# Performance work log

Hardware: AMD Instinct MI355X
Metric: run time of the kernel (lower is better)

## Reference

```python
import jax, jax.numpy as jnp
import numpy as np

N_HEADS = 16

def setup_inputs() -> dict:
    key = jax.random.key(0)
    k1, k2, k3 = jax.random.split(key, 3)
    d = 1024
    x = jax.random.normal(k1, (2, 2048, d), dtype=jnp.float32)
    W_in = jax.random.normal(k2, (d, 3 * d), dtype=jnp.float32) * (d ** -0.5)
    W_out = jax.random.normal(k3, (d, d), dtype=jnp.float32) * (d ** -0.5)
    return {"x": x, "W_in": W_in, "W_out": W_out}

def reference(x, W_in, W_out):
    B, S, D = x.shape
    H = N_HEADS
    Dh = D // H
    qkv = x @ W_in                                  # [B,S,3D]
    q, k, v = jnp.split(qkv, 3, axis=-1)
    # [B,S,D] -> [B,H,S,Dh]
    q = q.reshape(B, S, H, Dh).transpose(0, 2, 1, 3)
    k = k.reshape(B, S, H, Dh).transpose(0, 2, 1, 3)
    v = v.reshape(B, S, H, Dh).transpose(0, 2, 1, 3)
    scores = jnp.einsum('bhqd,bhkd->bhqk', q, k)    # [B,H,S,S]
    causal = jnp.triu(jnp.ones((S, S), dtype=bool), k=1)
    scores = jnp.where(causal, -jnp.inf, scores)
    scores = scores / jnp.sqrt(jnp.asarray(Dh, scores.dtype))
    attn = jax.nn.softmax(scores, axis=-1)
    out = jnp.einsum('bhqk,bhkd->bhqd', attn, v)    # [B,H,S,Dh]
    out = out.transpose(0, 2, 1, 3).reshape(B, S, D)
    return out @ W_out
```

## Files before the change

### kernel.cpp

```cpp
#include <hip/hip_runtime.h>
#include <cstdint>
#include <cstddef>

typedef __bf16 bf16;
typedef bf16  bf16x4  __attribute__((ext_vector_type(4)));
typedef bf16  bf16x8  __attribute__((ext_vector_type(8)));
typedef float floatx4 __attribute__((ext_vector_type(4)));

#define BATCH 2
#define SEQ   2048
#define DIM   1024
#define NH    16
#define DH    64
#define D3    3072
#define MROWS 4096

__device__ __forceinline__ void gld16(void* lds, const void* gptr) {
  __builtin_amdgcn_global_load_lds(
      (const __attribute__((address_space(1))) unsigned int*)gptr,
      (__attribute__((address_space(3))) unsigned int*)lds, 16, 0, 0);
}

__global__ __launch_bounds__(256) void k_prep(const float4* __restrict__ x,
                                              bf16* __restrict__ xb,
                                              const float* __restrict__ Wi,
                                              bf16* __restrict__ wti,
                                              const float* __restrict__ Wo,
                                              bf16* __restrict__ wto) {
  __shared__ float tile[32][33];
  const int bid = blockIdx.x;
  if (bid < 4096) {
    int i = bid * 256 + threadIdx.x;
    float4 v = x[i];
    bf16x4 o;
    o.x = (bf16)v.x; o.y = (bf16)v.y; o.z = (bf16)v.z; o.w = (bf16)v.w;
    *(bf16x4*)(xb + (size_t)i * 4) = o;
    return;
  }
  const float* W; bf16* Wt; int N, id;
  if (bid < 7168) { W = Wi; Wt = wti; N = 3072; id = bid - 4096; }
  else            { W = Wo; Wt = wto; N = 1024; id = bid - 7168; }
  const int nb = N / 32;
  int n0 = (id % nb) * 32, k0 = (id / nb) * 32;
  int tx = threadIdx.x & 31, ty = threadIdx.x >> 5;
#pragma unroll
  for (int i = 0; i < 4; i++)
    tile[ty + i * 8][tx] = W[(size_t)(k0 + ty + i * 8) * N + n0 + tx];
  __syncthreads();
#pragma unroll
  for (int i = 0; i < 4; i++)
    Wt[(size_t)(n0 + ty + i * 8) * 1024 + k0 + tx] = (bf16)tile[tx][ty + i * 8];
}

__global__ __launch_bounds__(512, 2) void k_gemm256(const bf16* __restrict__ A,
                                                    const bf16* __restrict__ Bt,
                                                    bf16* __restrict__ qk,
                                                    bf16* __restrict__ vt) {
  constexpr int K = DIM;
  constexpr int nk = K / 64;
  __shared__ __align__(16) bf16 As[2][256 * 64];
  __shared__ __align__(16) bf16 Bs[2][256 * 64];

  const int t = threadIdx.x, l = t & 63, w = t >> 6;
  const int q = l >> 4, mm = l & 15;
  const int wm = w >> 2, wn = w & 3;

  int id = blockIdx.x;
  id = (id & 7) * 24 + (id >> 3);
  const int by = id / 12, bx = id % 12;
  const int m0 = by * 256, n0 = bx * 256;

  auto stA = [&](int T, int up) {
    const int bp = T & 1;
#pragma unroll
    for (int i = 0; i < 2; i++) {
      int c = t + i * 512;
      int row = ((c >> 9) << 7) + (up << 6) + ((c >> 3) & 63);
      int pos = c & 7;
      int gs = pos ^ (row & 7);
      gld16((char*)(As[bp] + row * 64 + pos * 8),
            A + (size_t)(m0 + row) * K + T * 64 + gs * 8);
    }
  };
  auto stB = [&](int T, int up) {
    const int bp = T & 1;
#pragma unroll
    for (int i = 0; i < 2; i++) {
      int c = t + i * 512;
      int row = ((c >> 8) << 6) + (up << 5) + ((c >> 3) & 31);
      int pos = c & 7;
      int gs = pos ^ (row & 7);
      gld16((char*)(Bs[bp] + row * 64 + pos * 8),
            Bt + (size_t)(n0 + row) * K + T * 64 + gs * 8);
    }
  };

  floatx4 acc[8][4] = {};

  stA(0, 0); stB(0, 0); stA(0, 1); stB(0, 1);
  stA(1, 0); stB(1, 0);

  for (int T = 0; T < nk; T++) {
    const int bp = T & 1;
    if (T + 1 < nk)
      asm volatile("s_waitcnt vmcnt(4)\n\ts_barrier" ::: "memory");
    else
      asm volatile("s_waitcnt vmcnt(0)\n\ts_barrier" ::: "memory");

    const bf16* Ab = As[bp] + (size_t)(wm * 128) * 64;
    const bf16* Bb = Bs[bp] + (size_t)(wn * 64) * 64;
    bf16x8 af[4][2], bf0[2][2], bf1[2][2];

    if (T + 1 < nk) stA(T + 1, 1);
#pragma unroll
    for (int mt = 0; mt < 4; mt++)
#pragma unroll
      for (int kk = 0; kk < 2; kk++)
        af[mt][kk] = *(const bf16x8*)(Ab + (size_t)(mt * 16 + mm) * 64 +
                                      ((kk * 4 + q) ^ (mm & 7)) * 8);
#pragma unroll
    for (int nt = 0; nt < 2; nt++)
#pragma unroll
      for (int kk = 0; kk < 2; kk++)
        bf0[nt][kk] = *(const bf16x8*)(Bb + (size_t)(nt * 16 + mm) * 64 +
                                       ((kk * 4 + q) ^ (mm & 7)) * 8);
    asm volatile("s_barrier" ::: "memory");
    __builtin_amdgcn_s_setprio(1);
#pragma unroll
    for (int mt = 0; mt < 4; mt++)
#pragma unroll
      for (int nt = 0; nt < 2; nt++)
#pragma unroll
        for (int kk = 0; kk < 2; kk++)
          acc[mt][nt] = __builtin_amdgcn_mfma_f32_16x16x32_bf16(
              af[mt][kk], bf0[nt][kk], acc[mt][nt], 0, 0, 0);
    __builtin_amdgcn_s_setprio(0);
    asm volatile("s_barrier" ::: "memory");

    if (T + 1 < nk) stB(T + 1, 1);
#pragma unroll
    for (int nt = 0; nt < 2; nt++)
#pragma unroll
      for (int kk = 0; kk < 2; kk++)
        bf1[nt][kk] = *(const bf16x8*)(Bb + (size_t)(32 + nt * 16 + mm) * 64 +
                                       ((kk * 4 + q) ^ (mm & 7)) * 8);
    asm volatile("s_barrier" ::: "memory");
    __builtin_amdgcn_s_setprio(1);
#pragma unroll
    for (int mt = 0; mt < 4; mt++)
#pragma unroll
      for (int nt = 0; nt < 2; nt++)
#pragma unroll
        for (int kk = 0; kk < 2; kk++)
          acc[mt][2 + nt] = __builtin_amdgcn_mfma_f32_16x16x32_bf16(
              af[mt][kk], bf1[nt][kk], acc[mt][2 + nt], 0, 0, 0);
    __builtin_amdgcn_s_setprio(0);
    asm volatile("s_barrier" ::: "memory");

    if (T + 2 < nk) stA(T + 2, 0);
#pragma unroll
    for (int mt = 0; mt < 4; mt++)
#pragma unroll
      for (int kk = 0; kk < 2; kk++)
        af[mt][kk] = *(const bf16x8*)(Ab + (size_t)(64 + mt * 16 + mm) * 64 +
                                      ((kk * 4 + q) ^ (mm & 7)) * 8);
    asm volatile("s_barrier" ::: "memory");
    __builtin_amdgcn_s_setprio(1);
#pragma unroll
    for (int mt = 0; mt < 4; mt++)
#pragma unroll
      for (int nt = 0; nt < 2; nt++)
#pragma unroll
        for (int kk = 0; kk < 2; kk++)
          acc[4 + mt][nt] = __builtin_amdgcn_mfma_f32_16x16x32_bf16(
              af[mt][kk], bf0[nt][kk], acc[4 + mt][nt], 0, 0, 0);
    __builtin_amdgcn_s_setprio(0);
    asm volatile("s_barrier" ::: "memory");

    if (T + 2 < nk) stB(T + 2, 0);
    asm volatile("s_barrier" ::: "memory");
    __builtin_amdgcn_s_setprio(1);
#pragma unroll
    for (int mt = 0; mt < 4; mt++)
#pragma unroll
      for (int nt = 0; nt < 2; nt++)
#pragma unroll
        for (int kk = 0; kk < 2; kk++)
          acc[4 + mt][2 + nt] = __builtin_amdgcn_mfma_f32_16x16x32_bf16(
              af[mt][kk], bf1[nt][kk], acc[4 + mt][2 + nt], 0, 0, 0);
    __builtin_amdgcn_s_setprio(0);
  }

#pragma unroll
  for (int mt = 0; mt < 8; mt++)
#pragma unroll
    for (int nt = 0; nt < 4; nt++) {
      int row = m0 + wm * 128 + mt * 16 + q * 4;
      int col = n0 + wn * 64 + nt * 16 + mm;
      if (col < 2048) {
#pragma unroll
        for (int r = 0; r < 4; r++)
          qk[(size_t)(row + r) * 2048 + col] = (bf16)acc[mt][nt][r];
      } else {
        int d = col - 2048;
        int hh = d >> 6, dh = d & 63;
#pragma unroll
        for (int r = 0; r < 4; r++) {
          int rr = row + r;
          int bb = rr >> 11, s = rr & 2047;
          vt[((size_t)(bb * 16 + hh) * 64 + dh) * SEQ + s] = (bf16)acc[mt][nt][r];
        }
      }
    }
}

template <typename OutT, int MODE, int BN>
__global__ __launch_bounds__(256) void k_gemm_bt(const bf16* __restrict__ A,
                                                 const bf16* __restrict__ Bt,
                                                 OutT* __restrict__ C,
                                                 bf16* __restrict__ qk,
                                                 bf16* __restrict__ vt,
                                                 int M, int N, int K) {
  constexpr int LN = 2 + BN / 64;
  __shared__ __align__(16) bf16 As[3][128 * 32];
  __shared__ __align__(16) bf16 Bs[3][BN * 32];
  const int t = threadIdx.x, l = t & 63, w = t >> 6;
  const int q = l >> 4, mm = l & 15;
  const int m0 = blockIdx.y * 128, n0 = blockIdx.x * BN;
  constexpr int MT = (BN == 128) ? 4 : 2;
  const int mo = (BN == 128) ? ((w >> 1) * 64) : (w * 32);
  const int no = (BN == 128) ? ((w & 1) * 64) : 0;
  const int sw = (mm >> 1) & 3;

  auto stage = [&](int kt) {
    const int bp = kt % 3;
#pragma unroll
    for (int i = 0; i < 2; i++) {
      int c = t + i * 256;
      int row = c >> 2, pos = c & 3;
      int gs = pos ^ ((row >> 1) & 3);
      gld16((char*)As[bp] + (size_t)c * 16, A + (size_t)(m0 + row) * K + kt * 32 + gs * 8);
    }
#pragma unroll
    for (int i = 0; i < BN / 64; i++) {
      int c = t + i * 256;
      int row = c >> 2, pos = c & 3;
      int gs = pos ^ ((row >> 1) & 3);
      gld16((char*)Bs[bp] + (size_t)c * 16, Bt + (size_t)(n0 + row) * K + kt * 32 + gs * 8);
    }
  };

  floatx4 acc[MT][4] = {};
  const int nk = K >> 5;

  stage(0);
  stage(1);

  for (int kt = 0; kt < nk; kt++) {
    if (kt + 1 < nk)
      asm volatile("s_waitcnt vmcnt(%0)\n\ts_barrier" :: "n"(LN) : "memory");
    else
      asm volatile("s_waitcnt vmcnt(0)\n\ts_barrier" ::: "memory");
    if (kt + 2 < nk) stage(kt + 2);

    const bf16* Ab = As[kt % 3];
    const bf16* Bb = Bs[kt % 3];
    bf16x8 af[MT], bfr[4];
#pragma unroll
    for (int mt = 0; mt < MT; mt++)
      af[mt] = *(const bf16x8*)(Ab + (size_t)(mo + mt * 16 + mm) * 32 + (q ^ sw) * 8);
#pragma unroll
    for (int nt = 0; nt < 4; nt++)
      bfr[nt] = *(const bf16x8*)(Bb + (size_t)(no + nt * 16 + mm) * 32 + (q ^ sw) * 8);
#pragma unroll
    for (int mt = 0; mt < MT; mt++)
#pragma unroll
      for (int nt = 0; nt < 4; nt++)
        acc[mt][nt] = __builtin_amdgcn_mfma_f32_16x16x32_bf16(af[mt], bfr[nt],
                                                              acc[mt][nt], 0, 0, 0);
  }
#pragma unroll
  for (int mt = 0; mt < MT; mt++)
#pragma unroll
    for (int nt = 0; nt < 4; nt++)
#pragma unroll
      for (int r = 0; r < 4; r++) {
        int row = m0 + mo + mt * 16 + q * 4 + r;
        int col = n0 + no + nt * 16 + mm;
        if (MODE == 0) {
          C[(size_t)row * N + col] = (OutT)acc[mt][nt][r];
        } else {
          if (col < 2048) {
            qk[(size_t)row * 2048 + col] = (bf16)acc[mt][nt][r];
          } else {
            int d = col - 2048;
            int hh = d >> 6, dh = d & 63;
            int bb = row >> 11, s = row & 2047;
            vt[((size_t)(bb * 16 + hh) * 64 + dh) * SEQ + s] = (bf16)acc[mt][nt][r];
          }
        }
      }
}

__global__ __launch_bounds__(256, 4) void k_attn(const bf16* __restrict__ qk,
                                                 const bf16* __restrict__ vt,
                                                 bf16* __restrict__ out) {
  const int bx = blockIdx.x;
  const int qt = 31 - (bx >> 5);
  const int bh = bx & 31;
  const int b = bh >> 4, h = bh & 15;
  const int t = threadIdx.x, l = t & 63, w = t >> 6;
  const int q4 = l >> 4, mm = l & 15;
  const int sw = (mm >> 1) & 3;

  __shared__ __align__(16) char lds[8192 + 16384 + 16384];
  bf16* Qs = (bf16*)lds;
  bf16* Ps = (bf16*)lds;
  bf16* Ks = (bf16*)(lds + 8192);
  bf16* Vs = (bf16*)(lds + 8192 + 16384);

  const size_t qkbase = (size_t)b * SEQ * 2048;
  const size_t vtbase = (size_t)bh * 64 * SEQ;

  auto stage = [&](int kt) {
    const int bp = kt & 1;
#pragma unroll
    for (int i = 0; i < 2; i++) {
      int row = t >> 2, pos = t & 3;
      int g = pos ^ ((row >> 1) & 3);
      gld16((char*)(Ks + bp * 4096) + ((size_t)t + i * 256) * 16,
            qk + qkbase + (size_t)(kt * 64 + row) * 2048 + 1024 + h * 64 + i * 32 + g * 8);
    }
#pragma unroll
    for (int i = 0; i < 2; i++) {
      int c = t + i * 256;
      int vr = c >> 3, vc = c & 7;
      int src = vc ^ (vr & 7);
      gld16((char*)(Vs + bp * 4096) + (size_t)c * 16,
            vt + vtbase + (size_t)vr * SEQ + kt * 64 + src * 8);
    }
  };

  {
    int row = t >> 2, col = (t & 3) * 8;
#pragma unroll
    for (int i = 0; i < 2; i++)
      gld16((char*)Qs + ((size_t)t + i * 256) * 16,
            qk + qkbase + (size_t)(qt * 64 + row) * 2048 + h * 64 + i * 32 + col);
  }
  stage(0);
  __syncthreads();
  bf16x8 qf[2];
#pragma unroll
  for (int ks = 0; ks < 2; ks++) {
    qf[ks] = *(const bf16x8*)(Qs + (size_t)(ks * 64 + w * 16 + mm) * 32 + q4 * 8);
#pragma unroll
    for (int j = 0; j < 8; j++)
      qf[ks][j] = (bf16)((float)qf[ks][j] * 0.18033688f);
  }
  __syncthreads();

  float l_i = 0.f;
  floatx4 oaccT[4] = {};
  const int qloc = w * 16 + mm;
  const float FM = 24.0f;

  bf16* Pw = Ps + (size_t)w * 640;

  for (int kt = 0; kt <= qt; kt++) {
    if (kt < qt) stage(kt + 1);
    const bf16* Kb = Ks + (kt & 1) * 4096;
    const bf16* Vb = Vs + (kt & 1) * 4096;

    floatx4 sacc[4] = {};
#pragma unroll
    for (int ks = 0; ks < 2; ks++)
#pragma unroll
      for (int ct = 0; ct < 4; ct++) {
        bf16x8 kf = *(const bf16x8*)(Kb + (size_t)(ks * 64 + ct * 16 + mm) * 32 + (q4 ^ sw) * 8);
        sacc[ct] = __builtin_amdgcn_mfma_f32_16x16x32_bf16(kf, qf[ks], sacc[ct], 0, 0, 0);
      }

    bf16x4 pk[4];
    float rsum = 0.f;
    if (kt == qt) {
#pragma unroll
      for (int ct = 0; ct < 4; ct++)
#pragma unroll
        for (int r = 0; r < 4; r++) {
          float e = (ct * 16 + q4 * 4 + r > qloc)
                        ? 0.f : __builtin_amdgcn_exp2f(sacc[ct][r] - FM);
          pk[ct][r] = (bf16)e;
          rsum += e;
        }
    } else {
#pragma unroll
      for (int ct = 0; ct < 4; ct++)
#pragma unroll
        for (int r = 0; r < 4; r++) {
          float e = __builtin_amdgcn_exp2f(sacc[ct][r] - FM);
          pk[ct][r] = (bf16)e;
          rsum += e;
        }
    }
    rsum += __shfl_xor(rsum, 16, 64);
    rsum += __shfl_xor(rsum, 32, 64);
    l_i += rsum;

#pragma unroll
    for (int ks = 0; ks < 2; ks++) {
      *(bf16x4*)(Pw + (size_t)mm * 40 + q4 * 4)      = pk[ks * 2 + 0];
      *(bf16x4*)(Pw + (size_t)mm * 40 + 16 + q4 * 4) = pk[ks * 2 + 1];
      bf16x8 pf = *(const bf16x8*)(Pw + (size_t)mm * 40 + q4 * 8);
#pragma unroll
      for (int nt = 0; nt < 4; nt++) {
        int chunk = (ks * 4 + q4) ^ (mm & 7);
        bf16x8 vf = *(const bf16x8*)(Vb + (size_t)(nt * 16 + mm) * 64 + chunk * 8);
        oaccT[nt] = __builtin_amdgcn_mfma_f32_16x16x32_bf16(vf, pf, oaccT[nt], 0, 0, 0);
      }
    }

    if (kt < qt) __syncthreads();
  }

  float inv = 1.0f / l_i;
  int qrow = qt * 64 + qloc;
  bf16* orow = out + ((size_t)b * SEQ + qrow) * DIM + h * 64;
#pragma unroll
  for (int nt = 0; nt < 4; nt++) {
    bf16x4 o4;
#pragma unroll
    for (int r = 0; r < 4; r++) o4[r] = (bf16)(oaccT[nt][r] * inv);
    *(bf16x4*)(orow + nt * 16 + q4 * 4) = o4;
  }
}

extern "C" void kernel_launch(void* const* d_in, const int* in_sizes, int n_in,
                              void* d_out, int out_size, void* d_ws, size_t ws_size,
                              hipStream_t stream) {
  const float* x     = (const float*)d_in[0];
  const float* W_in  = (const float*)d_in[1];
  const float* W_out = (const float*)d_in[2];
  float* out = (float*)d_out;

  char* ws = (char*)d_ws;
  bf16* xb   = (bf16*)(ws);
  bf16* wti  = (bf16*)(ws + 8388608);
  bf16* wto  = (bf16*)(ws + 14680064);
  bf16* qkb  = (bf16*)(ws + 16777216);
  bf16* vtb  = (bf16*)(ws + 33554432);
  bf16* attn = xb;

  k_prep<<<8192, 256, 0, stream>>>((const float4*)x, xb, W_in, wti, W_out, wto);
  k_gemm256<<<192, 512, 0, stream>>>(xb, wti, qkb, vtb);
  k_attn<<<1024, 256, 0, stream>>>(qkb, vtb, attn);
  k_gemm_bt<float, 0, 64><<<dim3(16, 32), 256, 0, stream>>>(attn, wto, out, nullptr, nullptr,
                                                            MROWS, DIM, DIM);
}
```

Before: 183.7 us.

## Retile QKV GEMM to 128x192 blocks with 256 threads and XCD-aware mapping

Replaces the 256x256-tile, 512-thread QKV projection GEMM with a 128x192-tile, 256-thread kernel launched as 512 blocks, mapping block ids so that each XCD gets a contiguous 8x8 patch of tiles. The goal is to fill all CUs better (192 blocks underfilled the device) and keep L2 reuse local per XCD. In exchange each tile reuses data less and loads more operand bytes per FLOP. The staggered load/MFMA phases are kept, with the LDS reads moved ahead of the async global-to-LDS issue.

```diff
diff --git a/kernel.cpp b/kernel.cpp
--- a/kernel.cpp
+++ b/kernel.cpp
@@ -52,31 +52,31 @@
     Wt[(size_t)(n0 + ty + i * 8) * 1024 + k0 + tx] = (bf16)tile[tx][ty + i * 8];
 }
 
-__global__ __launch_bounds__(512, 2) void k_gemm256(const bf16* __restrict__ A,
-                                                    const bf16* __restrict__ Bt,
-                                                    bf16* __restrict__ qk,
-                                                    bf16* __restrict__ vt) {
+__global__ __launch_bounds__(256, 2) void k_gemm1(const bf16* __restrict__ A,
+                                                  const bf16* __restrict__ Bt,
+                                                  bf16* __restrict__ qk,
+                                                  bf16* __restrict__ vt) {
   constexpr int K = DIM;
   constexpr int nk = K / 64;
-  __shared__ __align__(16) bf16 As[2][256 * 64];
-  __shared__ __align__(16) bf16 Bs[2][256 * 64];
+  __shared__ __align__(16) bf16 As[2][128 * 64];
+  __shared__ __align__(16) bf16 Bs[2][192 * 64];
 
   const int t = threadIdx.x, l = t & 63, w = t >> 6;
   const int q = l >> 4, mm = l & 15;
-  const int wm = w >> 2, wn = w & 3;
-
-  int id = blockIdx.x;
-  id = (id & 7) * 24 + (id >> 3);
-  const int by = id / 12, bx = id % 12;
-  const int m0 = by * 256, n0 = bx * 256;
+  const int wm = w >> 1, wn = w & 1;
+
+  const int xcd = blockIdx.x & 7, j = blockIdx.x >> 3;
+  const int by = ((xcd >> 1) << 3) + (j >> 3);
+  const int bx = ((xcd & 1) << 3) + (j & 7);
+  const int m0 = by * 128, n0 = bx * 192;
 
   auto stA = [&](int T, int up) {
     const int bp = T & 1;
 #pragma unroll
     for (int i = 0; i < 2; i++) {
-      int c = t + i * 512;
-      int row = ((c >> 9) << 7) + (up << 6) + ((c >> 3) & 63);
-      int pos = c & 7;
+      int c = t + i * 256;
+      int rl = c >> 3, pos = c & 7;
+      int row = ((rl >> 5) << 6) + (up << 5) + (rl & 31);
       int gs = pos ^ (row & 7);
       gld16((char*)(As[bp] + row * 64 + pos * 8),
             A + (size_t)(m0 + row) * K + T * 64 + gs * 8);
@@ -85,17 +85,17 @@
   auto stB = [&](int T, int up) {
     const int bp = T & 1;
 #pragma unroll
-    for (int i = 0; i < 2; i++) {
-      int c = t + i * 512;
-      int row = ((c >> 8) << 6) + (up << 5) + ((c >> 3) & 31);
-      int pos = c & 7;
+    for (int i = 0; i < 3; i++) {
+      int c = t + i * 256;
+      int rl = c >> 3, pos = c & 7;
+      int row = up * 96 + rl;
       int gs = pos ^ (row & 7);
       gld16((char*)(Bs[bp] + row * 64 + pos * 8),
             Bt + (size_t)(n0 + row) * K + T * 64 + gs * 8);
     }
   };
 
-  floatx4 acc[8][4] = {};
+  floatx4 acc[4][6] = {};
 
   stA(0, 0); stB(0, 0); stA(0, 1); stB(0, 1);
   stA(1, 0); stB(1, 0);
@@ -103,100 +103,100 @@
   for (int T = 0; T < nk; T++) {
     const int bp = T & 1;
     if (T + 1 < nk)
-      asm volatile("s_waitcnt vmcnt(4)\n\ts_barrier" ::: "memory");
+      asm volatile("s_waitcnt vmcnt(5)\n\ts_barrier" ::: "memory");
     else
       asm volatile("s_waitcnt vmcnt(0)\n\ts_barrier" ::: "memory");
 
-    const bf16* Ab = As[bp] + (size_t)(wm * 128) * 64;
-    const bf16* Bb = Bs[bp] + (size_t)(wn * 64) * 64;
-    bf16x8 af[4][2], bf0[2][2], bf1[2][2];
-
+    const bf16* Ab = As[bp] + wm * 64 * 64;
+    const bf16* Bb = Bs[bp] + wn * 96 * 64;
+    bf16x8 a0[2][2], a1[2][2], b0[3][2], b1[3][2];
+
+#pragma unroll
+    for (int mt = 0; mt < 2; mt++)
+#pragma unroll
+      for (int kk = 0; kk < 2; kk++)
+        a0[mt][kk] = *(const bf16x8*)(Ab + (size_t)(mt * 16 + mm) * 64 +
+                                      ((kk * 4 + q) ^ (mm & 7)) * 8);
+#pragma unroll
+    for (int nt = 0; nt < 3; nt++)
+#pragma unroll
+      for (int kk = 0; kk < 2; kk++)
+        b0[nt][kk] = *(const bf16x8*)(Bb + (size_t)(nt * 16 + mm) * 64 +
+                                      ((kk * 4 + q) ^ (mm & 7)) * 8);
     if (T + 1 < nk) stA(T + 1, 1);
-#pragma unroll
-    for (int mt = 0; mt < 4; mt++)
-#pragma unroll
-      for (int kk = 0; kk < 2; kk++)
-        af[mt][kk] = *(const bf16x8*)(Ab + (size_t)(mt * 16 + mm) * 64 +
-                                      ((kk * 4 + q) ^ (mm & 7)) * 8);
-#pragma unroll
-    for (int nt = 0; nt < 2; nt++)
-#pragma unroll
-      for (int kk = 0; kk < 2; kk++)
-        bf0[nt][kk] = *(const bf16x8*)(Bb + (size_t)(nt * 16 + mm) * 64 +
-                                       ((kk * 4 + q) ^ (mm & 7)) * 8);
     asm volatile("s_barrier" ::: "memory");
     __builtin_amdgcn_s_setprio(1);
 #pragma unroll
-    for (int mt = 0; mt < 4; mt++)
-#pragma unroll
-      for (int nt = 0; nt < 2; nt++)
+    for (int mt = 0; mt < 2; mt++)
+#pragma unroll
+      for (int nt = 0; nt < 3; nt++)
 #pragma unroll
         for (int kk = 0; kk < 2; kk++)
           acc[mt][nt] = __builtin_amdgcn_mfma_f32_16x16x32_bf16(
-              af[mt][kk], bf0[nt][kk], acc[mt][nt], 0, 0, 0);
+              a0[mt][kk], b0[nt][kk], acc[mt][nt], 0, 0, 0);
     __builtin_amdgcn_s_setprio(0);
     asm volatile("s_barrier" ::: "memory");
 
+#pragma unroll
+    for (int nt = 0; nt < 3; nt++)
+#pragma unroll
+      for (int kk = 0; kk < 2; kk++)
+        b1[nt][kk] = *(const bf16x8*)(Bb + (size_t)((3 + nt) * 16 + mm) * 64 +
+                                      ((kk * 4 + q) ^ (mm & 7)) * 8);
     if (T + 1 < nk) stB(T + 1, 1);
-#pragma unroll
-    for (int nt = 0; nt < 2; nt++)
+    asm volatile("s_barrier" ::: "memory");
+    __builtin_amdgcn_s_setprio(1);
+#pragma unroll
+    for (int mt = 0; mt < 2; mt++)
+#pragma unroll
+      for (int nt = 0; nt < 3; nt++)
+#pragma unroll
+        for (int kk = 0; kk < 2; kk++)
+          acc[mt][3 + nt] = __builtin_amdgcn_mfma_f32_16x16x32_bf16(
+              a0[mt][kk], b1[nt][kk], acc[mt][3 + nt], 0, 0, 0);
+    __builtin_amdgcn_s_setprio(0);
+    asm volatile("s_barrier" ::: "memory");
+
+#pragma unroll
+    for (int mt = 0; mt < 2; mt++)
 #pragma unroll
       for (int kk = 0; kk < 2; kk++)
-        bf1[nt][kk] = *(const bf16x8*)(Bb + (size_t)(32 + nt * 16 + mm) * 64 +
-                                       ((kk * 4 + q) ^ (mm & 7)) * 8);
+        a1[mt][kk] = *(const bf16x8*)(Ab + (size_t)(32 + mt * 16 + mm) * 64 +
+                                      ((kk * 4 + q) ^ (mm & 7)) * 8);
+    if (T + 2 < nk) stA(T + 2, 0);
     asm volatile("s_barrier" ::: "memory");
     __builtin_amdgcn_s_setprio(1);
 #pragma unroll
-    for (int mt = 0; mt < 4; mt++)
-#pragma unroll
-      for (int nt = 0; nt < 2; nt++)
+    for (int mt = 0; mt < 2; mt++)
+#pragma unroll
+      for (int nt = 0; nt < 3; nt++)
 #pragma unroll
         for (int kk = 0; kk < 2; kk++)
-          acc[mt][2 + nt] = __builtin_amdgcn_mfma_f32_16x16x32_bf16(
-              af[mt][kk], bf1[nt][kk], acc[mt][2 + nt], 0, 0, 0);
+          acc[2 + mt][nt] = __builtin_amdgcn_mfma_f32_16x16x32_bf16(
+              a1[mt][kk], b0[nt][kk], acc[2 + mt][nt], 0, 0, 0);
     __builtin_amdgcn_s_setprio(0);
     asm volatile("s_barrier" ::: "memory");
 
-    if (T + 2 < nk) stA(T + 2, 0);
-#pragma unroll
-    for (int mt = 0; mt < 4; mt++)
-#pragma unroll
-      for (int kk = 0; kk < 2; kk++)
-        af[mt][kk] = *(const bf16x8*)(Ab + (size_t)(64 + mt * 16 + mm) * 64 +
-                                      ((kk * 4 + q) ^ (mm & 7)) * 8);
+    if (T + 2 < nk) stB(T + 2, 0);
     asm volatile("s_barrier" ::: "memory");
     __builtin_amdgcn_s_setprio(1);
 #pragma unroll
-    for (int mt = 0; mt < 4; mt++)
-#pragma unroll
-      for (int nt = 0; nt < 2; nt++)
+    for (int mt = 0; mt < 2; mt++)
+#pragma unroll
+      for (int nt = 0; nt < 3; nt++)
 #pragma unroll
         for (int kk = 0; kk < 2; kk++)
-          acc[4 + mt][nt] = __builtin_amdgcn_mfma_f32_16x16x32_bf16(
-              af[mt][kk], bf0[nt][kk], acc[4 + mt][nt], 0, 0, 0);
+          acc[2 + mt][3 + nt] = __builtin_amdgcn_mfma_f32_16x16x32_bf16(
+              a1[mt][kk], b1[nt][kk], acc[2 + mt][3 + nt], 0, 0, 0);
     __builtin_amdgcn_s_setprio(0);
-    asm volatile("s_barrier" ::: "memory");
-
-    if (T + 2 < nk) stB(T + 2, 0);
-    asm volatile("s_barrier" ::: "memory");
-    __builtin_amdgcn_s_setprio(1);
-#pragma unroll
-    for (int mt = 0; mt < 4; mt++)
-#pragma unroll
-      for (int nt = 0; nt < 2; nt++)
-#pragma unroll
-        for (int kk = 0; kk < 2; kk++)
-          acc[4 + mt][2 + nt] = __builtin_amdgcn_mfma_f32_16x16x32_bf16(
-              af[mt][kk], bf1[nt][kk], acc[4 + mt][2 + nt], 0, 0, 0);
-    __builtin_amdgcn_s_setprio(0);
-  }
-
-#pragma unroll
-  for (int mt = 0; mt < 8; mt++)
-#pragma unroll
-    for (int nt = 0; nt < 4; nt++) {
-      int row = m0 + wm * 128 + mt * 16 + q * 4;
-      int col = n0 + wn * 64 + nt * 16 + mm;
+  }
+
+#pragma unroll
+  for (int mt = 0; mt < 4; mt++)
+#pragma unroll
+    for (int nt = 0; nt < 6; nt++) {
+      int row = m0 + wm * 64 + mt * 16 + q * 4;
+      int col = n0 + wn * 96 + nt * 16 + mm;
       if (col < 2048) {
 #pragma unroll
         for (int r = 0; r < 4; r++)
@@ -452,7 +452,7 @@
   bf16* attn = xb;
 
   k_prep<<<8192, 256, 0, stream>>>((const float4*)x, xb, W_in, wti, W_out, wto);
-  k_gemm256<<<192, 512, 0, stream>>>(xb, wti, qkb, vtb);
+  k_gemm1<<<512, 256, 0, stream>>>(xb, wti, qkb, vtb);
   k_attn<<<1024, 256, 0, stream>>>(qkb, vtb, attn);
   k_gemm_bt<float, 0, 64><<<dim3(16, 32), 256, 0, stream>>>(attn, wto, out, nullptr, nullptr,
                                                             MROWS, DIM, DIM);
```

New measurement: 163.3 us. -11.1%, faster.
